# Kernel tuning notes

Hardware: AMD Instinct MI355X
Metric: run time of the kernel (lower is better)

The kernel has to match this reference:

```python
import jax, jax.numpy as jnp
import numpy as np

N = 500_000
E = 8_000_000
DIM = 3
CG_ITERS = 20
CG_TOL = 1e-4


def setup_inputs() -> dict:
    key = jax.random.key(0)
    k0, k1, k2, k3, k4, k5 = jax.random.split(key, 6)
    u_hat = jax.random.normal(k0, (N, DIM), dtype=jnp.float32)
    edge_index = jax.random.randint(k1, (2, E), 0, N, dtype=jnp.int32)
    face_normals = jax.random.normal(k2, (E, DIM), dtype=jnp.float32)
    face_areas = jax.random.uniform(k3, (E,), dtype=jnp.float32)
    face_dists = jax.random.uniform(k4, (E,), dtype=jnp.float32)
    cell_volumes = jax.random.uniform(k5, (N,), dtype=jnp.float32)
    return {
        "u_hat": u_hat,
        "edge_index": edge_index,
        "face_normals": face_normals,
        "face_areas": face_areas,
        "face_dists": face_dists,
        "cell_volumes": cell_volumes,
    }


def _segsum(vals, idx, n):
    return jax.ops.segment_sum(vals, idx, num_segments=n)


def reference(u_hat, edge_index, face_normals, face_areas, face_dists, cell_volumes):
    src, dst = edge_index[0], edge_index[1]
    n = u_hat.shape[0]

    # --- compute_divergence: D_i = (1/V_i) sum flux over faces into i ---
    u_face = 0.5 * (u_hat[src] + u_hat[dst])                 # (E, dim)
    flux = jnp.sum(u_face * face_normals, axis=-1) * face_areas  # (E,)
    div = _segsum(flux, dst, n) / jnp.clip(cell_volumes, 1e-12)

    # --- build_laplacian_rhs ---
    w = face_areas / jnp.clip(face_dists, 1e-8)              # (E,)
    diag = _segsum(w, dst, n)                                # (N,)
    off = -w
    b = div

    # --- cg_solve with Jacobi preconditioner ---
    m_inv = 1.0 / jnp.clip(diag, 1e-8)

    def matvec(phi):
        return diag * phi + _segsum(off * phi[src], dst, n)

    phi0 = jnp.zeros_like(b)
    r0 = b - matvec(phi0)
    z0 = m_inv * r0
    p0 = z0
    rz0 = jnp.sum(r0 * z0)

    def step(state, _):
        phi, r, z, p, rz, done = state
        # torch checks ||r|| < tol and breaks before the update
        active = jnp.logical_and(~done, jnp.linalg.norm(r) >= CG_TOL)
        ap = matvec(p)
        alpha = rz / (jnp.sum(p * ap) + 1e-12)
        phi_n = phi + alpha * p
        r_n = r - alpha * ap
        z_n = m_inv * r_n
        rz_n = jnp.sum(r_n * z_n)
        beta = rz_n / (rz + 1e-12)
        p_n = z_n + beta * p
        sel = lambda a, b_: jnp.where(active, a, b_)
        new_state = (sel(phi_n, phi), sel(r_n, r), sel(z_n, z),
                     sel(p_n, p), jnp.where(active, rz_n, rz), ~active)
        return new_state, None

    (phi, _, _, _, _, _), _ = jax.lax.scan(
        step, (phi0, r0, z0, p0, rz0, jnp.array(False)), None, length=CG_ITERS)

    # --- apply_pressure_correction ---
    grad_term = (w * phi[src])[:, None] * face_normals       # (E, dim)
    grad_phi = _segsum(grad_term, dst, n) / jnp.clip(cell_volumes, 1e-12)[:, None]
    u_corrected = u_hat - grad_phi
    return u_corrected, phi
```

## Files before the change

### kernel.cpp

```cpp
#include <hip/hip_runtime.h>


#define TPB 256
#define TPB_A 1024
#define TPB_B 1024
#define KB 2048
#define NBLK 256
#define BSHIFT 10
#define BSIZE 1024
#define MAXNB 512
#define CG_ITERS 20
#define TOL2 1e-8f

typedef unsigned long long ull;

struct Sum3 { float a, b, c; };

template <int BS>
__device__ inline Sum3 block_sum3n_bcast(const float* __restrict__ A, int nA,
                                         const float* __restrict__ B, int nB,
                                         const float* __restrict__ C, int nC) {
  float va = 0.f, vb = 0.f, vc = 0.f;
  for (int k = threadIdx.x; k < nA; k += BS) va += A[k];
  for (int k = threadIdx.x; k < nB; k += BS) vb += B[k];
  for (int k = threadIdx.x; k < nC; k += BS) vc += C[k];
#pragma unroll
  for (int o = 32; o; o >>= 1) {
    va += __shfl_down(va, o, 64);
    vb += __shfl_down(vb, o, 64);
    vc += __shfl_down(vc, o, 64);
  }
  __shared__ float sa[BS / 64], sb[BS / 64], sc[BS / 64], bc[3];
  int lane = threadIdx.x & 63, wid = threadIdx.x >> 6;
  if (lane == 0) { sa[wid] = va; sb[wid] = vb; sc[wid] = vc; }
  __syncthreads();
  if (threadIdx.x == 0) {
    float ta = 0.f, tb = 0.f, tc = 0.f;
#pragma unroll
    for (int k = 0; k < BS / 64; k++) { ta += sa[k]; tb += sb[k]; tc += sc[k]; }
    bc[0] = ta; bc[1] = tb; bc[2] = tc;
  }
  __syncthreads();
  Sum3 r{bc[0], bc[1], bc[2]};
  __syncthreads();
  return r;
}

template <int BS>
__device__ inline void block_reduce1_store(float v1, float* d1) {
#pragma unroll
  for (int o = 32; o; o >>= 1) v1 += __shfl_down(v1, o, 64);
  __shared__ float s1[BS / 64];
  int lane = threadIdx.x & 63, wid = threadIdx.x >> 6;
  if (lane == 0) s1[wid] = v1;
  __syncthreads();
  if (threadIdx.x == 0) {
    float t1 = 0.f;
#pragma unroll
    for (int k = 0; k < BS / 64; k++) t1 += s1[k];
    *d1 = t1;
  }
}

template <int BS>
__device__ inline void block_reduce2_store(float v1, float v2, float* d1, float* d2) {
#pragma unroll
  for (int o = 32; o; o >>= 1) {
    v1 += __shfl_down(v1, o, 64);
    v2 += __shfl_down(v2, o, 64);
  }
  __shared__ float s1[BS / 64], s2[BS / 64];
  int lane = threadIdx.x & 63, wid = threadIdx.x >> 6;
  if (lane == 0) { s1[wid] = v1; s2[wid] = v2; }
  __syncthreads();
  if (threadIdx.x == 0) {
    float t1 = 0.f, t2 = 0.f;
#pragma unroll
    for (int k = 0; k < BS / 64; k++) { t1 += s1[k]; t2 += s2[k]; }
    *d1 = t1;
    *d2 = t2;
  }
}

__global__ __launch_bounds__(TPB_A) void hist_wf(
    const int* __restrict__ ei, const float* __restrict__ u_hat,
    const float* __restrict__ fn, const float* __restrict__ fa,
    const float* __restrict__ fd, unsigned* __restrict__ mat,
    float2* __restrict__ wf, int E, int NB, int chunk) {
  __shared__ unsigned cntL[MAXNB];
  for (int i = threadIdx.x; i < NB; i += TPB_A) cntL[i] = 0;
  __syncthreads();
  int blk = blockIdx.x;
  int e0 = blk * chunk, e1 = min(E, e0 + chunk);
  for (int e = e0 + threadIdx.x; e < e1; e += TPB_A) {
    int d = ei[E + e];
    atomicAdd(&cntL[((unsigned)d) >> BSHIFT], 1u);
    if (wf) {
      int s = ei[e];
      float area = fa[e];
      float w = area / fmaxf(fd[e], 1e-8f);
      float ux = 0.5f * (u_hat[3 * s]     + u_hat[3 * d]);
      float uy = 0.5f * (u_hat[3 * s + 1] + u_hat[3 * d + 1]);
      float uz = 0.5f * (u_hat[3 * s + 2] + u_hat[3 * d + 2]);
      float flux = (ux * fn[3 * e] + uy * fn[3 * e + 1] + uz * fn[3 * e + 2]) * area;
      wf[e] = make_float2(w, flux);
    }
  }
  __syncthreads();
  for (int b = threadIdx.x; b < NB; b += TPB_A)
    mat[(size_t)b * NBLK + blk] = cntL[b];
}

__global__ __launch_bounds__(TPB) void scan_blocks(
    const unsigned* __restrict__ cnt, unsigned* __restrict__ offs,
    unsigned* __restrict__ btot, int n) {
  __shared__ unsigned sd[TPB];
  int t = threadIdx.x;
  int base = blockIdx.x * 1024 + t * 4;
  unsigned v0 = 0, v1 = 0, v2 = 0, v3 = 0;
  if (base + 0 < n) v0 = cnt[base + 0];
  if (base + 1 < n) v1 = cnt[base + 1];
  if (base + 2 < n) v2 = cnt[base + 2];
  if (base + 3 < n) v3 = cnt[base + 3];
  unsigned local = v0 + v1 + v2 + v3;
  sd[t] = local;
  __syncthreads();
  for (int o = 1; o < TPB; o <<= 1) {
    unsigned x = (t >= o) ? sd[t - o] : 0u;
    __syncthreads();
    sd[t] += x;
    __syncthreads();
  }
  unsigned excl = sd[t] - local;
  if (base + 0 < n) offs[base + 0] = excl; excl += v0;
  if (base + 1 < n) offs[base + 1] = excl; excl += v1;
  if (base + 2 < n) offs[base + 2] = excl; excl += v2;
  if (base + 3 < n) offs[base + 3] = excl;
  if (t == TPB - 1) btot[blockIdx.x] = sd[TPB - 1];
}

__global__ __launch_bounds__(512) void scan_totals(unsigned* __restrict__ btot, int nb) {
  __shared__ unsigned sd[512];
  int t = threadIdx.x;
  unsigned v = (t < nb) ? btot[t] : 0u;
  sd[t] = v;
  __syncthreads();
  for (int o = 1; o < 512; o <<= 1) {
    unsigned x = (t >= o) ? sd[t - o] : 0u;
    __syncthreads();
    sd[t] += x;
    __syncthreads();
  }
  if (t < nb) btot[t] = sd[t] - v;
}

__global__ __launch_bounds__(TPB) void scan_add(
    unsigned* __restrict__ offs, const unsigned* __restrict__ btot,
    int n, unsigned total) {
  int i = blockIdx.x * TPB + threadIdx.x;
  if (i < n) offs[i] += btot[i >> 10];
  if (i == 0) offs[n] = total;
}

__global__ __launch_bounds__(TPB_A) void bucket_place(
    const int* __restrict__ ei, const float* __restrict__ u_hat,
    const float* __restrict__ fn, const float* __restrict__ fa,
    const float* __restrict__ fd, const float2* __restrict__ wf,
    const unsigned* __restrict__ offs, uint4* __restrict__ A16,
    int E, int NB, int chunk) {
  __shared__ unsigned cntL[MAXNB];
  __shared__ unsigned offL[MAXNB];
  int blk = blockIdx.x;
  for (int i = threadIdx.x; i < NB; i += TPB_A) {
    cntL[i] = 0;
    offL[i] = offs[(size_t)i * NBLK + blk];
  }
  __syncthreads();
  int e0 = blk * chunk, e1 = min(E, e0 + chunk);
  for (int e = e0 + threadIdx.x; e < e1; e += TPB_A) {
    int s = ei[e], d = ei[E + e];
    float w, flux;
    if (wf) {
      float2 v = wf[e];
      w = v.x; flux = v.y;
    } else {
      float area = fa[e];
      w = area / fmaxf(fd[e], 1e-8f);
      float ux = 0.5f * (u_hat[3 * s]     + u_hat[3 * d]);
      float uy = 0.5f * (u_hat[3 * s + 1] + u_hat[3 * d + 1]);
      float uz = 0.5f * (u_hat[3 * s + 2] + u_hat[3 * d + 2]);
      flux = (ux * fn[3 * e] + uy * fn[3 * e + 1] + uz * fn[3 * e + 2]) * area;
    }
    unsigned b = ((unsigned)d) >> BSHIFT;
    unsigned dl = ((unsigned)d) & (BSIZE - 1u);
    unsigned r = atomicAdd(&cntL[b], 1u);
    unsigned pos = offL[b] + r;
    unsigned hi = (dl << 19) | (unsigned)s;
    A16[(size_t)pos] = make_uint4(hi, __float_as_uint(w),
                                  __float_as_uint(flux), (unsigned)e);
  }
}

__global__ __launch_bounds__(TPB_B) void node_setup(
    const uint4* __restrict__ A16, ull* __restrict__ A8,
    const unsigned* __restrict__ offs, const float* __restrict__ cv,
    float* __restrict__ diag, float* __restrict__ minv,
    float* __restrict__ r, float* __restrict__ z, float* __restrict__ phi,
    float* __restrict__ rz_part, float* __restrict__ rr_part, int N, int NB) {
  __shared__ float wacc[TPB_B], facc[TPB_B];
  int b = blockIdx.x;
  float rzv = 0.f, rrv = 0.f;
  if (b < NB) {
    wacc[threadIdx.x] = 0.f;
    facc[threadIdx.x] = 0.f;
    __syncthreads();
    unsigned jb = offs[(size_t)b * NBLK], je = offs[(size_t)(b + 1) * NBLK];
    const ull* q = (const ull*)A16;
    for (unsigned j = jb + threadIdx.x; j < je; j += TPB_B) {
      ull a = __builtin_nontemporal_load(&q[(size_t)2 * j]);
      ull bq = __builtin_nontemporal_load(&q[(size_t)2 * j + 1]);
      unsigned hi = (unsigned)a;
      float w = __uint_as_float((unsigned)(a >> 32));
      float flux = __uint_as_float((unsigned)bq);
      atomicAdd(&wacc[hi >> 19], w);
      atomicAdd(&facc[hi >> 19], flux);
      if (A8) A8[(size_t)j] = a;
    }
    __syncthreads();
    int node = (b << BSHIFT) + threadIdx.x;
    if (node < N) {
      float wsum = wacc[threadIdx.x];
      float vol = fmaxf(cv[node], 1e-12f);
      float bval = facc[threadIdx.x] / vol;
      float mi = 1.0f / fmaxf(wsum, 1e-8f);
      diag[node] = wsum;
      minv[node] = mi;
      r[node] = bval;
      float zi = mi * bval;
      z[node] = zi;
      phi[node] = 0.f;
      rzv = bval * zi;
      rrv = bval * bval;
    }
  }
  block_reduce2_store<TPB_B>(rzv, rrv, &rz_part[blockIdx.x], &rr_part[blockIdx.x]);
}

__global__ __launch_bounds__(TPB_B) void matvec_az(
    const float* __restrict__ z, const float* __restrict__ diag,
    const unsigned* __restrict__ offs, const ull* __restrict__ A8,
    const uint4* __restrict__ A16,
    const float* __restrict__ p_old, float* __restrict__ p_new,
    const float* __restrict__ ap_old, float* __restrict__ ap_new,
    float* __restrict__ pap_part,
    const float* __restrict__ rzJ_part, const float* __restrict__ rzJm1_part,
    const float* __restrict__ rrJ_part, int N, int first) {
  __shared__ float acc[TPB_B];
  int b = blockIdx.x;
  acc[threadIdx.x] = 0.f;
  __syncthreads();
  unsigned jb = offs[(size_t)b * NBLK], je = offs[(size_t)(b + 1) * NBLK];
  if (A8) {
    for (unsigned j = jb + threadIdx.x; j < je; j += TPB_B) {
      ull v = __builtin_nontemporal_load(&A8[(size_t)j]);
      unsigned hi = (unsigned)v;
      float w = __uint_as_float((unsigned)(v >> 32));
      atomicAdd(&acc[hi >> 19], w * z[hi & 0x7FFFFu]);
    }
  } else {
    const ull* q = (const ull*)A16;
    for (unsigned j = jb + threadIdx.x; j < je; j += TPB_B) {
      ull v = __builtin_nontemporal_load(&q[(size_t)2 * j]);
      unsigned hi = (unsigned)v;
      float w = __uint_as_float((unsigned)(v >> 32));
      atomicAdd(&acc[hi >> 19], w * z[hi & 0x7FFFFu]);
    }
  }
  __syncthreads();
  float beta = 0.f;
  bool act = true;
  if (!first) {
    Sum3 s = block_sum3n_bcast<TPB_B>(rzJ_part, KB, rzJm1_part, KB, rrJ_part, KB);
    act = (s.c >= TOL2);
    beta = s.a / (s.b + 1e-12f);
  }
  float contrib = 0.f;
  int node = (b << BSHIFT) + threadIdx.x;
  if (node < N) {
    float zi = z[node];
    float az = diag[node] * zi - acc[threadIdx.x];
    float pn, apn;
    if (first)    { pn = zi;                          apn = az; }
    else if (act) { pn = fmaf(beta, p_old[node], zi); apn = fmaf(beta, ap_old[node], az); }
    else          { pn = p_old[node];                 apn = ap_old[node]; }
    p_new[node] = pn;
    ap_new[node] = apn;
    contrib = pn * apn;
  }
  block_reduce1_store<TPB_B>(contrib, &pap_part[b]);
}

__global__ __launch_bounds__(TPB) void cg_update(
    float* __restrict__ phi, float* __restrict__ r, const float* __restrict__ p,
    const float* __restrict__ ap, const float* __restrict__ minv,
    float* __restrict__ z,
    const float* __restrict__ pap_it, const float* __restrict__ rz_it,
    const float* __restrict__ rr_it, float* __restrict__ rz_next,
    float* __restrict__ rr_next, int N, int NB) {
  Sum3 s = block_sum3n_bcast<TPB>(pap_it, NB, rz_it, KB, rr_it, KB);
  bool act = (s.c >= TOL2);
  float alpha = s.b / (s.a + 1e-12f);
  float rzacc = 0.f, rracc = 0.f;
  for (int i = blockIdx.x * TPB + threadIdx.x; i < N; i += KB * TPB) {
    float ri = r[i];
    if (act) {
      phi[i] += alpha * p[i];
      ri -= alpha * ap[i];
      r[i] = ri;
    }
    float zi = minv[i] * ri;
    z[i] = zi;
    rzacc += ri * zi;
    rracc += ri * ri;
  }
  block_reduce2_store<TPB>(rzacc, rracc, &rz_next[blockIdx.x], &rr_next[blockIdx.x]);
}

__global__ __launch_bounds__(TPB_B) void finalize(
    const float* __restrict__ u_hat, const float* __restrict__ cv,
    const float* __restrict__ phi, const unsigned* __restrict__ offs,
    const uint4* __restrict__ A16, const float* __restrict__ fn,
    float* __restrict__ out, int N, int NB) {
  __shared__ float gxa[TPB_B], gya[TPB_B], gza[TPB_B];
  int b = blockIdx.x;
  if (b >= NB) return;
  gxa[threadIdx.x] = 0.f;
  gya[threadIdx.x] = 0.f;
  gza[threadIdx.x] = 0.f;
  __syncthreads();
  unsigned jb = offs[(size_t)b * NBLK], je = offs[(size_t)(b + 1) * NBLK];
  const ull* q = (const ull*)A16;
  for (unsigned j = jb + threadIdx.x; j < je; j += TPB_B) {
    ull a = __builtin_nontemporal_load(&q[(size_t)2 * j]);
    ull bq = __builtin_nontemporal_load(&q[(size_t)2 * j + 1]);
    unsigned hi = (unsigned)a;
    float w = __uint_as_float((unsigned)(a >> 32));
    int e = (int)(unsigned)(bq >> 32);
    float t = w * phi[hi & 0x7FFFFu];
    int dl = hi >> 19;
    atomicAdd(&gxa[dl], t * fn[3 * e]);
    atomicAdd(&gya[dl], t * fn[3 * e + 1]);
    atomicAdd(&gza[dl], t * fn[3 * e + 2]);
  }
  __syncthreads();
  int node = (b << BSHIFT) + threadIdx.x;
  if (node < N) {
    float iv = 1.0f / fmaxf(cv[node], 1e-12f);
    out[3 * node]     = u_hat[3 * node]     - gxa[threadIdx.x] * iv;
    out[3 * node + 1] = u_hat[3 * node + 1] - gya[threadIdx.x] * iv;
    out[3 * node + 2] = u_hat[3 * node + 2] - gza[threadIdx.x] * iv;
    out[3 * N + node] = phi[node];
  }
}

extern "C" void kernel_launch(void* const* d_in, const int* in_sizes, int n_in,
                              void* d_out, int out_size, void* d_ws, size_t ws_size,
                              hipStream_t stream) {
  const float* u_hat = (const float*)d_in[0];
  const int*   ei    = (const int*)d_in[1];
  const float* fn    = (const float*)d_in[2];
  const float* fa    = (const float*)d_in[3];
  const float* fd    = (const float*)d_in[4];
  const float* cv    = (const float*)d_in[5];
  float* out = (float*)d_out;

  const int N = in_sizes[0] / 3;
  const int E = in_sizes[1] / 2;
  const int NB = (N + BSIZE - 1) >> BSHIFT;
  const int NS = NB * NBLK;
  const int chunk = (E + NBLK - 1) / NBLK;

  char* base = (char*)d_ws;
  size_t off = 0;
  auto alloc = [&](size_t bytes) -> void* {
    void* ptr = base + off;
    off = (off + bytes + 255) & ~size_t(255);
    return ptr;
  };
  unsigned* mat   = (unsigned*)alloc((size_t)NS * 4);
  unsigned* offs  = (unsigned*)alloc((size_t)(NS + 1) * 4);
  unsigned* btot  = (unsigned*)alloc(512 * 4);
  float*    diag  = (float*)alloc((size_t)N * 4);
  float*    minv  = (float*)alloc((size_t)N * 4);
  float*    phi   = (float*)alloc((size_t)N * 4);
  float*    rvec  = (float*)alloc((size_t)N * 4);
  float*    zvec  = (float*)alloc((size_t)N * 4);
  float*    pA    = (float*)alloc((size_t)N * 4);
  float*    pB    = (float*)alloc((size_t)N * 4);
  float*    apA   = (float*)alloc((size_t)N * 4);
  float*    apB   = (float*)alloc((size_t)N * 4);
  float*    rzrr  = (float*)alloc((size_t)(2 * (CG_ITERS + 1)) * KB * 4);
  float*    papp  = (float*)alloc((size_t)CG_ITERS * KB * 4);
  uint4*    A16   = (uint4*)alloc((size_t)E * 16);
  ull* A8 = nullptr;
  if (off + (size_t)E * 8 + 256 <= ws_size) A8 = (ull*)alloc((size_t)E * 8);
  float2* WF = nullptr;
  if (off + (size_t)E * 8 + 256 <= ws_size) WF = (float2*)alloc((size_t)E * 8);
  (void)n_in; (void)out_size;

  auto rz_part = [&](int it) { return rzrr + (size_t)(2 * it) * KB; };
  auto rr_part = [&](int it) { return rzrr + (size_t)(2 * it + 1) * KB; };
  auto pap_part = [&](int it) { return papp + (size_t)it * KB; };

  const int nbScan = (NS + 1023) / 1024;
  const int gridScanAdd = (NS + TPB - 1) / TPB;

  hist_wf<<<NBLK, TPB_A, 0, stream>>>(ei, u_hat, fn, fa, fd, mat, WF,
                                      E, NB, chunk);

  scan_blocks<<<nbScan, TPB, 0, stream>>>(mat, offs, btot, NS);
  scan_totals<<<1, 512, 0, stream>>>(btot, nbScan);
  scan_add<<<gridScanAdd, TPB, 0, stream>>>(offs, btot, NS, (unsigned)E);

  bucket_place<<<NBLK, TPB_A, 0, stream>>>(ei, u_hat, fn, fa, fd, WF, offs,
                                           A16, E, NB, chunk);

  node_setup<<<KB, TPB_B, 0, stream>>>(A16, A8, offs, cv, diag, minv,
                                       rvec, zvec, phi,
                                       rz_part(0), rr_part(0), N, NB);

  float* pbuf[2]  = {pA, pB};
  float* apbuf[2] = {apA, apB};
  for (int it = 0; it < CG_ITERS; it++) {
    int ni = it & 1;
    float* pn  = pbuf[ni];
    float* apn = apbuf[ni];
    const float* po  = pbuf[1 - ni];
    const float* apo = apbuf[1 - ni];
    int first = (it == 0) ? 1 : 0;
    matvec_az<<<NB, TPB_B, 0, stream>>>(zvec, diag, offs, A8, A16,
                                        po, pn, apo, apn, pap_part(it),
                                        rz_part(it), rz_part(it > 0 ? it - 1 : 0),
                                        rr_part(it), N, first);
    cg_update<<<KB, TPB, 0, stream>>>(phi, rvec, pn, apn, minv, zvec,
                                      pap_part(it), rz_part(it), rr_part(it),
                                      rz_part(it + 1), rr_part(it + 1), N, NB);
  }

  finalize<<<NB, TPB_B, 0, stream>>>(u_hat, cv, phi, offs, A16,
                                     fn, out, N, NB);
}
```

Baseline: 2.165 ms.

## Build per-row CSR in node_setup and use thread-per-row matvec without atomics

node_setup now counts edges per destination within each bucket, scans the counts in shared memory, and scatters the packed (weight, src) entries into a row-sorted A8 array with a rowptr. The CG matvec then has each thread walk its own row and accumulate in registers, two entries at a time, replacing the shared-memory atomicAdd accumulation and its block syncs. This adds a second pass over A16 and a rowptr array in setup, and per-row lengths vary, so thread-per-row can leave lanes in a wavefront uneven. Launch bounds for the matvec also request higher occupancy.

```diff
diff --git a/kernel.cpp b/kernel.cpp
--- a/kernel.cpp
+++ b/kernel.cpp
@@ -203,35 +203,61 @@
 
 __global__ __launch_bounds__(TPB_B) void node_setup(
     const uint4* __restrict__ A16, ull* __restrict__ A8,
+    unsigned* __restrict__ rowptr,
     const unsigned* __restrict__ offs, const float* __restrict__ cv,
     float* __restrict__ diag, float* __restrict__ minv,
     float* __restrict__ r, float* __restrict__ z, float* __restrict__ phi,
-    float* __restrict__ rz_part, float* __restrict__ rr_part, int N, int NB) {
+    float* __restrict__ rz_part, float* __restrict__ rr_part,
+    int N, int NB, int E) {
+  __shared__ unsigned cntS[TPB_B];
+  __shared__ unsigned scanS[TPB_B];
   __shared__ float wacc[TPB_B], facc[TPB_B];
   int b = blockIdx.x;
+  int t = threadIdx.x;
   float rzv = 0.f, rrv = 0.f;
   if (b < NB) {
-    wacc[threadIdx.x] = 0.f;
-    facc[threadIdx.x] = 0.f;
+    cntS[t] = 0; wacc[t] = 0.f; facc[t] = 0.f;
     __syncthreads();
     unsigned jb = offs[(size_t)b * NBLK], je = offs[(size_t)(b + 1) * NBLK];
     const ull* q = (const ull*)A16;
-    for (unsigned j = jb + threadIdx.x; j < je; j += TPB_B) {
+    for (unsigned j = jb + t; j < je; j += TPB_B) {
       ull a = __builtin_nontemporal_load(&q[(size_t)2 * j]);
-      ull bq = __builtin_nontemporal_load(&q[(size_t)2 * j + 1]);
+      ull c = __builtin_nontemporal_load(&q[(size_t)2 * j + 1]);
       unsigned hi = (unsigned)a;
-      float w = __uint_as_float((unsigned)(a >> 32));
-      float flux = __uint_as_float((unsigned)bq);
-      atomicAdd(&wacc[hi >> 19], w);
-      atomicAdd(&facc[hi >> 19], flux);
-      if (A8) A8[(size_t)j] = a;
-    }
-    __syncthreads();
-    int node = (b << BSHIFT) + threadIdx.x;
+      unsigned dl = hi >> 19;
+      atomicAdd(&cntS[dl], 1u);
+      atomicAdd(&wacc[dl], __uint_as_float((unsigned)(a >> 32)));
+      atomicAdd(&facc[dl], __uint_as_float((unsigned)c));
+    }
+    __syncthreads();
+    scanS[t] = cntS[t];
+    __syncthreads();
+    for (int o = 1; o < TPB_B; o <<= 1) {
+      unsigned x = (t >= o) ? scanS[t - o] : 0u;
+      __syncthreads();
+      scanS[t] += x;
+      __syncthreads();
+    }
+    unsigned baseE = scanS[t] - cntS[t];
+    __syncthreads();
+    scanS[t] = baseE;
+    cntS[t] = 0;
+    __syncthreads();
+    if (A8 && rowptr) {
+      for (unsigned j = jb + t; j < je; j += TPB_B) {
+        ull a = __builtin_nontemporal_load(&q[(size_t)2 * j]);
+        unsigned hi = (unsigned)a;
+        unsigned dl = hi >> 19, src = hi & 0x7FFFFu;
+        unsigned rk = atomicAdd(&cntS[dl], 1u);
+        unsigned pos = jb + scanS[dl] + rk;
+        A8[(size_t)pos] = (a & 0xFFFFFFFF00000000ull) | (ull)src;
+      }
+    }
+    int node = (b << BSHIFT) + t;
     if (node < N) {
-      float wsum = wacc[threadIdx.x];
+      float wsum = wacc[t];
       float vol = fmaxf(cv[node], 1e-12f);
-      float bval = facc[threadIdx.x] / vol;
+      float bval = facc[t] / vol;
       float mi = 1.0f / fmaxf(wsum, 1e-8f);
       diag[node] = wsum;
       minv[node] = mi;
@@ -239,44 +265,25 @@
       float zi = mi * bval;
       z[node] = zi;
       phi[node] = 0.f;
+      if (rowptr) rowptr[node] = jb + baseE;
       rzv = bval * zi;
       rrv = bval * bval;
     }
+    if (rowptr && b == NB - 1 && t == 0) rowptr[N] = (unsigned)E;
   }
   block_reduce2_store<TPB_B>(rzv, rrv, &rz_part[blockIdx.x], &rr_part[blockIdx.x]);
 }
 
-__global__ __launch_bounds__(TPB_B) void matvec_az(
+__global__ __launch_bounds__(TPB_B, 8) void matvec_az(
     const float* __restrict__ z, const float* __restrict__ diag,
     const unsigned* __restrict__ offs, const ull* __restrict__ A8,
-    const uint4* __restrict__ A16,
+    const unsigned* __restrict__ rowptr, const uint4* __restrict__ A16,
     const float* __restrict__ p_old, float* __restrict__ p_new,
     const float* __restrict__ ap_old, float* __restrict__ ap_new,
     float* __restrict__ pap_part,
     const float* __restrict__ rzJ_part, const float* __restrict__ rzJm1_part,
     const float* __restrict__ rrJ_part, int N, int first) {
-  __shared__ float acc[TPB_B];
-  int b = blockIdx.x;
-  acc[threadIdx.x] = 0.f;
-  __syncthreads();
-  unsigned jb = offs[(size_t)b * NBLK], je = offs[(size_t)(b + 1) * NBLK];
-  if (A8) {
-    for (unsigned j = jb + threadIdx.x; j < je; j += TPB_B) {
-      ull v = __builtin_nontemporal_load(&A8[(size_t)j]);
-      unsigned hi = (unsigned)v;
-      float w = __uint_as_float((unsigned)(v >> 32));
-      atomicAdd(&acc[hi >> 19], w * z[hi & 0x7FFFFu]);
-    }
-  } else {
-    const ull* q = (const ull*)A16;
-    for (unsigned j = jb + threadIdx.x; j < je; j += TPB_B) {
-      ull v = __builtin_nontemporal_load(&q[(size_t)2 * j]);
-      unsigned hi = (unsigned)v;
-      float w = __uint_as_float((unsigned)(v >> 32));
-      atomicAdd(&acc[hi >> 19], w * z[hi & 0x7FFFFu]);
-    }
-  }
-  __syncthreads();
+  int b = blockIdx.x, t = threadIdx.x;
   float beta = 0.f;
   bool act = true;
   if (!first) {
@@ -284,11 +291,44 @@
     act = (s.c >= TOL2);
     beta = s.a / (s.b + 1e-12f);
   }
+  int node = (b << BSHIFT) + t;
+  float accv = 0.f;
+  if (A8 && rowptr) {
+    if (node < N) {
+      unsigned r0 = rowptr[node], r1 = rowptr[node + 1];
+      unsigned j = r0;
+      for (; j + 1 < r1; j += 2) {
+        ull v0 = __builtin_nontemporal_load(&A8[(size_t)j]);
+        ull v1 = __builtin_nontemporal_load(&A8[(size_t)j + 1]);
+        float z0 = z[(unsigned)v0];
+        float z1 = z[(unsigned)v1];
+        accv = fmaf(__uint_as_float((unsigned)(v0 >> 32)), z0, accv);
+        accv = fmaf(__uint_as_float((unsigned)(v1 >> 32)), z1, accv);
+      }
+      if (j < r1) {
+        ull v0 = __builtin_nontemporal_load(&A8[(size_t)j]);
+        accv = fmaf(__uint_as_float((unsigned)(v0 >> 32)), z[(unsigned)v0], accv);
+      }
+    }
+  } else {
+    __shared__ float accS[TPB_B];
+    accS[t] = 0.f;
+    __syncthreads();
+    unsigned jb = offs[(size_t)b * NBLK], je = offs[(size_t)(b + 1) * NBLK];
+    const ull* q = (const ull*)A16;
+    for (unsigned j = jb + t; j < je; j += TPB_B) {
+      ull v = __builtin_nontemporal_load(&q[(size_t)2 * j]);
+      unsigned hi = (unsigned)v;
+      float w = __uint_as_float((unsigned)(v >> 32));
+      atomicAdd(&accS[hi >> 19], w * z[hi & 0x7FFFFu]);
+    }
+    __syncthreads();
+    accv = accS[t];
+  }
   float contrib = 0.f;
-  int node = (b << BSHIFT) + threadIdx.x;
   if (node < N) {
     float zi = z[node];
-    float az = diag[node] * zi - acc[threadIdx.x];
+    float az = diag[node] * zi - accv;
     float pn, apn;
     if (first)    { pn = zi;                          apn = az; }
     else if (act) { pn = fmaf(beta, p_old[node], zi); apn = fmaf(beta, ap_old[node], az); }
@@ -399,6 +439,7 @@
   float*    pB    = (float*)alloc((size_t)N * 4);
   float*    apA   = (float*)alloc((size_t)N * 4);
   float*    apB   = (float*)alloc((size_t)N * 4);
+  unsigned* rowptr = (unsigned*)alloc((size_t)(N + 1) * 4);
   float*    rzrr  = (float*)alloc((size_t)(2 * (CG_ITERS + 1)) * KB * 4);
   float*    papp  = (float*)alloc((size_t)CG_ITERS * KB * 4);
   uint4*    A16   = (uint4*)alloc((size_t)E * 16);
@@ -425,9 +466,9 @@
   bucket_place<<<NBLK, TPB_A, 0, stream>>>(ei, u_hat, fn, fa, fd, WF, offs,
                                            A16, E, NB, chunk);
 
-  node_setup<<<KB, TPB_B, 0, stream>>>(A16, A8, offs, cv, diag, minv,
+  node_setup<<<KB, TPB_B, 0, stream>>>(A16, A8, rowptr, offs, cv, diag, minv,
                                        rvec, zvec, phi,
-                                       rz_part(0), rr_part(0), N, NB);
+                                       rz_part(0), rr_part(0), N, NB, E);
 
   float* pbuf[2]  = {pA, pB};
   float* apbuf[2] = {apA, apB};
@@ -438,7 +479,7 @@
     const float* po  = pbuf[1 - ni];
     const float* apo = apbuf[1 - ni];
     int first = (it == 0) ? 1 : 0;
-    matvec_az<<<NB, TPB_B, 0, stream>>>(zvec, diag, offs, A8, A16,
+    matvec_az<<<NB, TPB_B, 0, stream>>>(zvec, diag, offs, A8, rowptr, A16,
                                         po, pn, apo, apn, pap_part(it),
                                         rz_part(it), rz_part(it > 0 ? it - 1 : 0),
                                         rr_part(it), N, first);
```

Measured after the change: 3.356 ms. 1.55x slower.

## Halve node block size and vectorize edge record loads to 128-bit

Applied to the files above, without the earlier changes.

Shrinks the destination-node block from 1024 to 512 nodes (so twice as many blocks, up to 1024), and replaces paired 64-bit nontemporal loads of the packed edge records with single 128-bit vector loads. In the matvec, each thread now processes two 8-byte edges per 16-byte load, with scalar handling of an unaligned head and an odd tail. The aim is fewer memory instructions and better occupancy and parallelism in the edge-streaming kernels. It relies on the bucket layout, packed node bits and the offsets/partials arrays all staying consistent with the new BSHIFT and MAXNB.

```diff
diff --git a/kernel.cpp b/kernel.cpp
--- a/kernel.cpp
+++ b/kernel.cpp
@@ -3,16 +3,17 @@
 
 #define TPB 256
 #define TPB_A 1024
-#define TPB_B 1024
+#define TPB_B 512
 #define KB 2048
 #define NBLK 256
-#define BSHIFT 10
-#define BSIZE 1024
-#define MAXNB 512
+#define BSHIFT 9
+#define BSIZE 512
+#define MAXNB 1024
 #define CG_ITERS 20
 #define TOL2 1e-8f
 
 typedef unsigned long long ull;
+typedef ull v2u __attribute__((ext_vector_type(2)));
 
 struct Sum3 { float a, b, c; };
 
@@ -215,16 +216,15 @@
     facc[threadIdx.x] = 0.f;
     __syncthreads();
     unsigned jb = offs[(size_t)b * NBLK], je = offs[(size_t)(b + 1) * NBLK];
-    const ull* q = (const ull*)A16;
+    const v2u* Q = (const v2u*)A16;
     for (unsigned j = jb + threadIdx.x; j < je; j += TPB_B) {
-      ull a = __builtin_nontemporal_load(&q[(size_t)2 * j]);
-      ull bq = __builtin_nontemporal_load(&q[(size_t)2 * j + 1]);
-      unsigned hi = (unsigned)a;
-      float w = __uint_as_float((unsigned)(a >> 32));
-      float flux = __uint_as_float((unsigned)bq);
+      v2u a = __builtin_nontemporal_load(&Q[(size_t)j]);
+      unsigned hi = (unsigned)a[0];
+      float w = __uint_as_float((unsigned)(a[0] >> 32));
+      float flux = __uint_as_float((unsigned)a[1]);
       atomicAdd(&wacc[hi >> 19], w);
       atomicAdd(&facc[hi >> 19], flux);
-      if (A8) A8[(size_t)j] = a;
+      if (A8) A8[(size_t)j] = a[0];
     }
     __syncthreads();
     int node = (b << BSHIFT) + threadIdx.x;
@@ -256,23 +256,42 @@
     const float* __restrict__ rzJ_part, const float* __restrict__ rzJm1_part,
     const float* __restrict__ rrJ_part, int N, int first) {
   __shared__ float acc[TPB_B];
-  int b = blockIdx.x;
-  acc[threadIdx.x] = 0.f;
+  int b = blockIdx.x, t = threadIdx.x;
+  acc[t] = 0.f;
   __syncthreads();
   unsigned jb = offs[(size_t)b * NBLK], je = offs[(size_t)(b + 1) * NBLK];
   if (A8) {
-    for (unsigned j = jb + threadIdx.x; j < je; j += TPB_B) {
-      ull v = __builtin_nontemporal_load(&A8[(size_t)j]);
-      unsigned hi = (unsigned)v;
-      float w = __uint_as_float((unsigned)(v >> 32));
-      atomicAdd(&acc[hi >> 19], w * z[hi & 0x7FFFFu]);
+    unsigned jv = jb;
+    if (jb & 1u) {
+      if (t == 0 && jb < je) {
+        ull v = A8[(size_t)jb];
+        unsigned h = (unsigned)v;
+        atomicAdd(&acc[h >> 19], __uint_as_float((unsigned)(v >> 32)) * z[h & 0x7FFFFu]);
+      }
+      jv = jb + 1;
+    }
+    if (jv > je) jv = je;
+    unsigned npairs = (je - jv) >> 1;
+    const v2u* P = (const v2u*)(A8 + jv);
+    for (unsigned p = t; p < npairs; p += TPB_B) {
+      v2u v = __builtin_nontemporal_load(&P[(size_t)p]);
+      unsigned h0 = (unsigned)v[0], h1 = (unsigned)v[1];
+      float z0 = z[h0 & 0x7FFFFu];
+      float z1 = z[h1 & 0x7FFFFu];
+      atomicAdd(&acc[h0 >> 19], __uint_as_float((unsigned)(v[0] >> 32)) * z0);
+      atomicAdd(&acc[h1 >> 19], __uint_as_float((unsigned)(v[1] >> 32)) * z1);
+    }
+    if (((je - jv) & 1u) && t == 0) {
+      ull v = A8[(size_t)(je - 1)];
+      unsigned h = (unsigned)v;
+      atomicAdd(&acc[h >> 19], __uint_as_float((unsigned)(v >> 32)) * z[h & 0x7FFFFu]);
     }
   } else {
-    const ull* q = (const ull*)A16;
-    for (unsigned j = jb + threadIdx.x; j < je; j += TPB_B) {
-      ull v = __builtin_nontemporal_load(&q[(size_t)2 * j]);
-      unsigned hi = (unsigned)v;
-      float w = __uint_as_float((unsigned)(v >> 32));
+    const v2u* Q = (const v2u*)A16;
+    for (unsigned j = jb + t; j < je; j += TPB_B) {
+      v2u a = __builtin_nontemporal_load(&Q[(size_t)j]);
+      unsigned hi = (unsigned)a[0];
+      float w = __uint_as_float((unsigned)(a[0] >> 32));
       atomicAdd(&acc[hi >> 19], w * z[hi & 0x7FFFFu]);
     }
   }
@@ -285,10 +304,10 @@
     beta = s.a / (s.b + 1e-12f);
   }
   float contrib = 0.f;
-  int node = (b << BSHIFT) + threadIdx.x;
+  int node = (b << BSHIFT) + t;
   if (node < N) {
     float zi = z[node];
-    float az = diag[node] * zi - acc[threadIdx.x];
+    float az = diag[node] * zi - acc[t];
     float pn, apn;
     if (first)    { pn = zi;                          apn = az; }
     else if (act) { pn = fmaf(beta, p_old[node], zi); apn = fmaf(beta, ap_old[node], az); }
@@ -339,13 +358,12 @@
   gza[threadIdx.x] = 0.f;
   __syncthreads();
   unsigned jb = offs[(size_t)b * NBLK], je = offs[(size_t)(b + 1) * NBLK];
-  const ull* q = (const ull*)A16;
+  const v2u* Q = (const v2u*)A16;
   for (unsigned j = jb + threadIdx.x; j < je; j += TPB_B) {
-    ull a = __builtin_nontemporal_load(&q[(size_t)2 * j]);
-    ull bq = __builtin_nontemporal_load(&q[(size_t)2 * j + 1]);
-    unsigned hi = (unsigned)a;
-    float w = __uint_as_float((unsigned)(a >> 32));
-    int e = (int)(unsigned)(bq >> 32);
+    v2u a = __builtin_nontemporal_load(&Q[(size_t)j]);
+    unsigned hi = (unsigned)a[0];
+    float w = __uint_as_float((unsigned)(a[0] >> 32));
+    int e = (int)(unsigned)(a[1] >> 32);
     float t = w * phi[hi & 0x7FFFFu];
     int dl = hi >> 19;
     atomicAdd(&gxa[dl], t * fn[3 * e]);
```

Result: faster. 2.108 ms (-2.6%).
